# Performance work log

Measured on AMD Instinct MI355X. Metric: run time of the kernel, lower is better.

The kernel has to match this reference:

```python
import jax, jax.numpy as jnp
import numpy as np
import jax.scipy.linalg as jsp

H = 8
C = 64
D_CONV = 4
EPS_L2 = 1e-6
EPS_RMS = 1e-5


def l2norm(x):
    return x * jax.lax.rsqrt(jnp.sum(x * x, axis=-1, keepdims=True) + EPS_L2)


def setup_inputs() -> dict:
    key = jax.random.key(0)
    ks = jax.random.split(key, 12)
    B, T, D = 4, 4096, 1024
    x = jax.random.normal(ks[0], (B, T, D), dtype=jnp.float32)
    s = 0.02
    Wv = jax.random.normal(ks[1], (D, D), dtype=jnp.float32) * s
    Wg = jax.random.normal(ks[2], (D, D), dtype=jnp.float32) * s
    Wo = jax.random.normal(ks[3], (D, D), dtype=jnp.float32) * s
    Wb = jax.random.normal(ks[4], (H, D), dtype=jnp.float32) * s
    Wa = jax.random.normal(ks[5], (H, D), dtype=jnp.float32) * s
    # dt_bias / A_log initialized as in the torch module
    u = jax.random.uniform(ks[6], (H,))
    dt = jnp.exp(u * (jnp.log(0.1) - jnp.log(0.001)) + jnp.log(0.001))
    dt_bias = dt + jnp.log(-jnp.expm1(-dt))
    A_log = jnp.log(jax.random.uniform(ks[7], (H,)) * 16.0 + 1e-4)
    norm_w = jnp.ones((D // H,), dtype=jnp.float32)
    conv_w = jax.random.normal(ks[8], (D, D_CONV), dtype=jnp.float32) * 0.1
    conv_b = jnp.zeros((D,), dtype=jnp.float32)
    return {"x": x, "Wv": Wv, "Wg": Wg, "Wo": Wo, "Wb": Wb, "Wa": Wa,
            "dt_bias": dt_bias, "A_log": A_log, "norm_w": norm_w,
            "conv_w": conv_w, "conv_b": conv_b}


def _causal_depthwise_conv(x, w, b):
    # x: (B,T,D), w: (D,d_conv) -- causal depthwise conv1d
    B, T, D = x.shape
    xp = jnp.pad(x, ((0, 0), (D_CONV - 1, 0), (0, 0)))
    out = b
    for j in range(D_CONV):
        out = out + xp[:, j:j + T] * w[:, j]
    return out


def _forward(x, Wv, Wg, Wo, Wb, Wa, dt_bias, A_log, norm_w, conv_w, conv_b):
    B, T, D = x.shape
    K = D // H
    n = T // C  # T chosen as a multiple of C, so pad_len == 0

    rk = l2norm(x.reshape(B, T, H, K)) / np.sqrt(K)
    x_shift = jnp.pad(x[:, :-1], ((0, 0), (1, 0), (0, 0)))
    wk = l2norm(x_shift.reshape(B, T, H, K))
    v = jax.nn.silu(_causal_depthwise_conv(x @ Wv.T, conv_w, conv_b)).reshape(B, T, H, K)
    gate = (x @ Wg.T).reshape(B, T, H, K)
    beta = jax.nn.sigmoid(x @ Wb.T)                       # (B,T,H)
    decay = -jnp.exp(A_log) * jax.nn.softplus(x @ Wa.T + dt_bias)  # (B,T,H)

    # -> (B,H,T,K)
    rk, wk, v = (jnp.transpose(t, (0, 2, 1, 3)) for t in (rk, wk, v))
    beta_t = jnp.transpose(beta, (0, 2, 1))[..., None]    # (B,H,T,1)
    v = v * beta_t
    wk_beta = wk * beta_t

    # chunk: (B,H,n,C,K)
    ch = lambda t: t.reshape(B, H, n, C, K)
    rk, wk, v, wk_beta = ch(rk), ch(wk), ch(v), ch(wk_beta)
    decay = jnp.cumsum(jnp.transpose(decay, (0, 2, 1)).reshape(B, H, n, C), axis=-1)
    decay_exp = jnp.exp(decay)[..., None]                 # (B,H,n,C,1)

    tril = jnp.tril(jnp.ones((C, C), dtype=bool))
    strict_lower = jnp.tril(jnp.ones((C, C), dtype=bool), k=-1)
    diff = decay[..., :, None] - decay[..., None, :]
    L_mask = jnp.where(tril, jnp.exp(jnp.where(tril, diff, 0.0)), 0.0)  # (B,H,n,C,C)

    A_strict = jnp.where(strict_lower,
                         -(jnp.einsum('bhnck,bhndk->bhncd', wk_beta, wk) * L_mask), 0.0)
    # forward-substitution loop == inverse of unit-lower-triangular (I - A_strict)
    eye = jnp.eye(C, dtype=x.dtype)
    Tmat = jsp.solve_triangular(eye - A_strict,
                                jnp.broadcast_to(eye, A_strict.shape),
                                lower=True)
    v = Tmat @ v
    wk_cumdecay = Tmat @ (wk_beta * decay_exp)

    # scan over chunks maintaining state S: (B,H,K,K)
    def step(S, inp):
        rk_i, wk_i, v_i, wkc_i, L_i, dec_i = inp
        attn = jnp.where(tril, jnp.einsum('bhck,bhdk->bhcd', rk_i, wk_i) * L_i, 0.0)
        v_new = v_i - wkc_i @ S
        o_inter = (rk_i * jnp.exp(dec_i)[..., None]) @ S
        o_i = o_inter + attn @ v_new
        dw = jnp.exp(dec_i[..., -1:] - dec_i)[..., None]
        S_new = S * jnp.exp(dec_i[..., -1])[..., None, None] + \
            jnp.einsum('bhck,bhcv->bhkv', wk_i * dw, v_new)
        return S_new, o_i

    mv = lambda t: jnp.moveaxis(t, 2, 0)  # chunk axis to front
    S0 = jnp.zeros((B, H, K, K), dtype=x.dtype)
    _, o = jax.lax.scan(step, S0, (mv(rk), mv(wk), mv(v), mv(wk_cumdecay),
                                   mv(L_mask), mv(decay)))
    # o: (n,B,H,C,K) -> (B,T,H,K)
    o = jnp.transpose(o, (1, 0, 3, 2, 4)).reshape(B, T, H, K)

    # per-head RMSNorm, gated, output projection
    o = o * jax.lax.rsqrt(jnp.mean(o * o, axis=-1, keepdims=True) + EPS_RMS) * norm_w
    o = o * jax.nn.silu(gate)
    return o.reshape(B, T, D) @ Wo.T


def reference(x, Wv, Wg, Wo, Wb, Wa, dt_bias, A_log, norm_w, conv_w, conv_b):
    return _forward(x, Wv, Wg, Wo, Wb, Wa, dt_bias, A_log, norm_w, conv_w, conv_b)
```

## Files before the change

kernel.cpp:

```cpp
#include <hip/hip_runtime.h>
#include <hip/hip_bf16.h>
#include <math.h>

#define H_ 8
#define K_ 128
#define C_ 64
#define D_ 1024
#define T_ 4096
#define B_ 4
#define N_CH 64
#define BT_ (B_*T_)

typedef __attribute__((ext_vector_type(8))) short bf16x8;
typedef __attribute__((ext_vector_type(4))) float f32x4;
typedef __hip_bfloat16 bf16;

#define BAR_LGKM() do { \
  asm volatile("s_waitcnt lgkmcnt(0)" ::: "memory"); \
  __builtin_amdgcn_sched_barrier(0); \
  __builtin_amdgcn_s_barrier(); \
} while(0)

__device__ __forceinline__ float siluf(float x){ return x / (1.0f + expf(-x)); }
__device__ __forceinline__ float expn(float x){ return expf(fminf(x, 0.f)); }
__device__ __forceinline__ float sanf(float v){ return (__builtin_fabsf(v) <= 1e30f) ? v : 0.f; }

__device__ __forceinline__ void ld_bf4(const bf16* p, float* o){
  uint2 u = *(const uint2*)p;
  o[0]=__uint_as_float(u.x<<16); o[1]=__uint_as_float(u.x&0xffff0000u);
  o[2]=__uint_as_float(u.y<<16); o[3]=__uint_as_float(u.y&0xffff0000u);
}
__device__ __forceinline__ void ld_bf4s(const bf16* p, float* o){
  ld_bf4(p, o);
#pragma unroll
  for (int e=0;e<4;e++) o[e] = sanf(o[e]);
}
__device__ __forceinline__ unsigned short f2bfu(float f){
  bf16 h = __float2bfloat16(f);
  return *reinterpret_cast<unsigned short*>(&h);
}
__device__ __forceinline__ uint2 pack_bf4(const float* v){
  uint2 r;
  r.x = (unsigned)f2bfu(v[0]) | ((unsigned)f2bfu(v[1])<<16);
  r.y = (unsigned)f2bfu(v[2]) | ((unsigned)f2bfu(v[3])<<16);
  return r;
}
__device__ __forceinline__ bf16x8 u4_to_b8(uint4 u){
  union { uint4 u; bf16x8 b; } cv; cv.u = u; return cv.b;
}

template<int I> __device__ __forceinline__ void fsub_step(float* v, const float (*sa)[64]){
  const float* ar = sa[I];
  float s0=0.f,s1=0.f,s2=0.f,s3=0.f;
  constexpr int I4 = I & ~3;
#pragma unroll
  for (int j=0;j<I4;j+=4){
    float4 a4 = *(const float4*)&ar[j];
    s0 += a4.x*v[j+0]; s1 += a4.y*v[j+1]; s2 += a4.z*v[j+2]; s3 += a4.w*v[j+3];
  }
#pragma unroll
  for (int j=I4;j<I;j++) s0 += ar[j]*v[j];
  v[I] += (s0+s2)+(s1+s3);
}
template<int I> __device__ __forceinline__ void fsub_all(float* v, const float (*sa)[64]){
  if constexpr (I >= 1){
    fsub_all<I-1>(v, sa);
    fsub_step<I>(v, sa);
  }
}

__global__ __launch_bounds__(256) void cast_f2b(
    const float* __restrict__ src, bf16* __restrict__ dst, int n4)
{
  int i = blockIdx.x*256 + threadIdx.x;
  if (i >= n4) return;
  float4 v = *(const float4*)&src[(size_t)i*4];
  float a[4] = {v.x, v.y, v.z, v.w};
  *(uint2*)&dst[(size_t)i*4] = pack_bf4(a);
}

template<typename OUT_T, bool FUSE_NG>
__global__ __launch_bounds__(256) void gemm_bt_mfma(
    const bf16* __restrict__ X, const bf16* __restrict__ W,
    OUT_T* __restrict__ Y, int M, int N, int K,
    const bf16* __restrict__ o_in, const float* __restrict__ norm_w)
{
  __shared__ __align__(16) bf16 As[128*64];
  __shared__ __align__(16) bf16 Bs[128*64];
  const int tid = threadIdx.x;
  const int wv = tid >> 6;
  const int lane = tid & 63;
  const int row0 = blockIdx.y*128, col0 = blockIdx.x*128;
  const int mw = (wv&1)*64, nw = (wv>>1)*64;
  const int q = lane >> 4;
  const int l15 = lane & 15;
  const int swr = l15 & 7;
  f32x4 acc[4][4];
#pragma unroll
  for (int mi=0;mi<4;mi++)
#pragma unroll
    for (int ni=0;ni<4;ni++) acc[mi][ni] = (f32x4){0.f,0.f,0.f,0.f};

  const int sr8 = lane >> 3;
  const int scs = ((lane & 7) ^ sr8) * 8;
  for (int k0=0;k0<K;k0+=64){
#pragma unroll
    for (int i=0;i<4;i++){
      __builtin_amdgcn_global_load_lds(
          (const void*)&X[(size_t)(row0 + i*32 + wv*8 + sr8)*K + k0 + scs],
          (void*)&As[i*2048 + wv*512], 16, 0, 0);
      __builtin_amdgcn_global_load_lds(
          (const void*)&W[(size_t)(col0 + i*32 + wv*8 + sr8)*K + k0 + scs],
          (void*)&Bs[i*2048 + wv*512], 16, 0, 0);
    }
    __syncthreads();
#pragma unroll
    for (int ks=0; ks<64; ks+=32){
      bf16x8 af[4], bfr[4];
#pragma unroll
      for (int i=0;i<4;i++){
        const int cc = (((ks>>3) + q) ^ swr) * 8;
        af[i]  = *(const bf16x8*)&As[(mw + i*16 + l15)*64 + cc];
        bfr[i] = *(const bf16x8*)&Bs[(nw + i*16 + l15)*64 + cc];
      }
#pragma unroll
      for (int mi=0;mi<4;mi++)
#pragma unroll
        for (int ni=0;ni<4;ni++)
          acc[mi][ni] = __builtin_amdgcn_mfma_f32_16x16x32_bf16(af[mi], bfr[ni], acc[mi][ni], 0,0,0);
    }
    __syncthreads();
  }

  if constexpr (FUSE_NG){
    float* s_red = (float*)As;
    const int hh = blockIdx.x;
    const int nwh = nw >> 6;
#pragma unroll
    for (int mi=0;mi<4;mi++){
#pragma unroll
      for (int reg=0;reg<4;reg++){
        int row = row0 + mw + mi*16 + q*4 + reg;
        int b = row >> 12, t = row & (T_-1);
        const bf16* orow = o_in + ((size_t)(b*H_+hh)*T_ + t)*K_;
        float ps = 0.f;
#pragma unroll
        for (int ni=0;ni<4;ni++){
          float ov = sanf(__bfloat162float(orow[nw + ni*16 + l15]));
          ps += ov*ov;
        }
        ps += __shfl_xor(ps,1,64); ps += __shfl_xor(ps,2,64);
        ps += __shfl_xor(ps,4,64); ps += __shfl_xor(ps,8,64);
        if (l15 == 0) s_red[nwh*128 + mw + mi*16 + q*4 + reg] = ps;
      }
    }
    __syncthreads();
#pragma unroll
    for (int mi=0;mi<4;mi++){
#pragma unroll
      for (int reg=0;reg<4;reg++){
        int lr = mw + mi*16 + q*4 + reg;
        float ssum = s_red[lr] + s_red[128 + lr];
        float rr = rsqrtf(ssum*(1.f/128.f) + 1e-5f);
        int row = row0 + lr;
        int b = row >> 12, t = row & (T_-1);
        const bf16* orow = o_in + ((size_t)(b*H_+hh)*T_ + t)*K_;
#pragma unroll
        for (int ni=0;ni<4;ni++){
          int k = nw + ni*16 + l15;
          float ov = sanf(__bfloat162float(orow[k]));
          float res = ov * rr * norm_w[k] * siluf(acc[mi][ni][reg]);
          Y[(size_t)row*N + col0 + k] = (OUT_T)__float2bfloat16(res);
        }
      }
    }
  } else {
#pragma unroll
    for (int mi=0;mi<4;mi++){
#pragma unroll
      for (int reg=0;reg<4;reg++){
        int row = row0 + mw + mi*16 + q*4 + reg;
#pragma unroll
        for (int ni=0;ni<4;ni++){
          int col = col0 + nw + ni*16 + l15;
          if constexpr (sizeof(OUT_T) == 2)
            Y[(size_t)row*N + col] = (OUT_T)__float2bfloat16(acc[mi][ni][reg]);
          else
            Y[(size_t)row*N + col] = (OUT_T)acc[mi][ni][reg];
        }
      }
    }
  }
}

__global__ __launch_bounds__(256) void proj_small(
    const float* __restrict__ x, const float* __restrict__ Wb, const float* __restrict__ Wa,
    const float* __restrict__ dt_bias, const float* __restrict__ A_log,
    float* __restrict__ beta_out, float* __restrict__ dec_out)
{
  const int w = threadIdx.x >> 6;
  const int lane = threadIdx.x & 63;
  const int bt = blockIdx.x*4 + w;
  const int b = bt >> 12, t = bt & (T_-1);
  const float* xr = x + (size_t)bt*D_;
  float xv[16];
#pragma unroll
  for (int p=0;p<4;p++){
    float4 v = *(const float4*)&xr[lane*16 + p*4];
    xv[p*4+0]=v.x; xv[p*4+1]=v.y; xv[p*4+2]=v.z; xv[p*4+3]=v.w;
  }
  float accb[H_], acca[H_];
#pragma unroll
  for (int h=0;h<H_;h++){
    float sb=0.f, sa=0.f;
#pragma unroll
    for (int p=0;p<4;p++){
      float4 wb = *(const float4*)&Wb[(size_t)h*D_ + lane*16 + p*4];
      float4 wa = *(const float4*)&Wa[(size_t)h*D_ + lane*16 + p*4];
      sb += xv[p*4+0]*wb.x + xv[p*4+1]*wb.y + xv[p*4+2]*wb.z + xv[p*4+3]*wb.w;
      sa += xv[p*4+0]*wa.x + xv[p*4+1]*wa.y + xv[p*4+2]*wa.z + xv[p*4+3]*wa.w;
    }
    accb[h]=sb; acca[h]=sa;
  }
#pragma unroll
  for (int h=0;h<H_;h++){
#pragma unroll
    for (int m=1;m<64;m<<=1){
      accb[h] += __shfl_xor(accb[h], m, 64);
      acca[h] += __shfl_xor(acca[h], m, 64);
    }
  }
  if (lane < H_) {
    int h = lane;
    beta_out[(size_t)(b*H_+h)*T_ + t] = 1.f/(1.f+expf(-accb[h]));
  } else if (lane < 2*H_) {
    int h = lane - H_;
    float z = acca[h] + dt_bias[h];
    float sp = fmaxf(z,0.f) + log1pf(expf(-fabsf(z)));
    dec_out[(size_t)(b*H_+h)*T_ + t] = -expf(A_log[h]) * sp;
  }
}

__global__ __launch_bounds__(256) void xinv_kernel(
    const float* __restrict__ x, float* __restrict__ xinv, bf16* __restrict__ xb)
{
  const int bt = blockIdx.x;
  const int b = bt >> 12, t = bt & (T_-1);
  const int tid = threadIdx.x;
  float4 xv = *(const float4*)&x[(size_t)bt*D_ + tid*4];
  float a[4] = {xv.x, xv.y, xv.z, xv.w};
  *(uint2*)&xb[(size_t)bt*D_ + tid*4] = pack_bf4(a);
  float ss = xv.x*xv.x + xv.y*xv.y + xv.z*xv.z + xv.w*xv.w;
#pragma unroll
  for (int m=1;m<32;m<<=1) ss += __shfl_xor(ss, m, 32);
  const int h = tid >> 5;
  if ((tid & 31) == 0)
    xinv[(size_t)(b*H_+h)*T_ + t] = rsqrtf(ss + 1e-6f);
}

__global__ __launch_bounds__(256) void cumsum_dec(
    const float* __restrict__ dec_raw, float* __restrict__ dec_cum)
{
  int g = blockIdx.x*4 + (threadIdx.x>>6);
  int lane = threadIdx.x & 63;
  float v = sanf(dec_raw[(size_t)g*C_ + lane]);
#pragma unroll
  for (int off=1; off<64; off<<=1){
    float u = __shfl_up(v, off, 64);
    if (lane >= off) v += u;
  }
  dec_cum[(size_t)g*C_ + lane] = v;
}

__global__ __launch_bounds__(256) void chunk_prep(
    const bf16* __restrict__ xb, const float* __restrict__ xinv,
    const bf16* __restrict__ vpre, const float* __restrict__ cw, const float* __restrict__ cb,
    const float* __restrict__ beta, const float* __restrict__ dec,
    bf16* __restrict__ vchk, bf16* __restrict__ wkc, bf16* __restrict__ attn)
{
  __shared__ __align__(16) bf16 s_x[65][136];
  __shared__ __align__(16) float s_a[64][64];
  __shared__ float s_dec[64], s_beta[64], s_invsh[64], s_negbi[64], s_rsc[64], s_sc2[64];

  const int tid = threadIdx.x;
  const int chunk = blockIdx.x;
  const int bh = chunk >> 6;
  const int nc = chunk & 63;
  const int b = bh >> 3, h = bh & 7;
  const int t0 = nc * C_;
  const size_t xrow = (size_t)b*T_;
  const size_t rowb = (size_t)bh*T_ + t0;
  const size_t kobase = rowb * K_;
  const int w = tid >> 6;
  const int lane = tid & 63;
  const int l15 = lane & 15;
  const int q = lane >> 4;

  for (int idx = tid; idx < 65*16; idx += 256){
    int r = idx >> 4;
    int seg = (idx & 15) * 8;
    int t = t0 + r - 1;
    int tr = t < 0 ? 0 : t;
    *(uint4*)&s_x[r][seg] = *(const uint4*)&xb[(xrow + tr)*D_ + h*K_ + seg];
  }
  if (tid < C_){
    int c = tid;
    float dv  = sanf(dec[rowb + c]);
    float bet = sanf(beta[rowb + c]);
    float invc = sanf(xinv[rowb + c]);
    int tm1 = t0 + c - 1;
    float ivs = (tm1 >= 0) ? sanf(xinv[(size_t)bh*T_ + tm1]) : 0.f;
    s_dec[c] = dv;
    s_beta[c] = bet;
    s_invsh[c] = ivs;
    s_negbi[c] = -bet * ivs;
    s_rsc[c] = invc * 0.08838834764831845f;
    s_sc2[c] = ivs * bet * expn(dv);
  }
  __syncthreads();

  bf16x8 aG[4], aT[4];
#pragma unroll
  for (int ks=0; ks<4; ks++){
    aG[ks] = *(const bf16x8*)&s_x[16*w + l15][ks*32 + q*8];
    aT[ks] = *(const bf16x8*)&s_x[16*w + l15 + 1][ks*32 + q*8];
  }
  f32x4 accG[4], accT[4];
#pragma unroll
  for (int J=0;J<4;J++){ accG[J]=(f32x4){0.f,0.f,0.f,0.f}; accT[J]=(f32x4){0.f,0.f,0.f,0.f}; }
#pragma unroll
  for (int J=0;J<4;J++){
    if (J <= w){
#pragma unroll
      for (int ks=0; ks<4; ks++){
        bf16x8 bfrag = *(const bf16x8*)&s_x[16*J + l15][ks*32 + q*8];
        accG[J] = __builtin_amdgcn_mfma_f32_16x16x32_bf16(aG[ks], bfrag, accG[J], 0,0,0);
        accT[J] = __builtin_amdgcn_mfma_f32_16x16x32_bf16(aT[ks], bfrag, accT[J], 0,0,0);
      }
    }
  }
  {
    const int i0 = 16*w + q*4;
#pragma unroll
    for (int J=0;J<4;J++){
      const int j = 16*J + l15;
#pragma unroll
      for (int reg=0;reg<4;reg++){
        const int i = i0 + reg;
        if (j < i)
          s_a[i][j] = s_negbi[i] * s_invsh[j] * expn(s_dec[i]-s_dec[j]) * accG[J][reg];
        float val = 0.f;
        if (j <= i)
          val = s_rsc[i] * s_invsh[j] * expn(s_dec[i]-s_dec[j]) * accT[J][reg];
        attn[(size_t)chunk*4096 + i*64 + j] = __float2bfloat16(val);
      }
    }
  }

  float v[64];
  if (tid < 128){
    const int col = tid;
    float4 cwv = *(const float4*)&cw[(h*K_+col)*4];
    const float cbv = cb[h*K_+col];
    const bf16* vp = vpre + (xrow + t0)*D_ + h*K_ + col;
    float win0, win1, win2;
    { int t = t0-3; win0 = (t>=0)? sanf(__bfloat162float(vpre[(xrow+t)*D_+h*K_+col])) : 0.f; }
    { int t = t0-2; win1 = (t>=0)? sanf(__bfloat162float(vpre[(xrow+t)*D_+h*K_+col])) : 0.f; }
    { int t = t0-1; win2 = (t>=0)? sanf(__bfloat162float(vpre[(xrow+t)*D_+h*K_+col])) : 0.f; }
#pragma unroll
    for (int c8=0; c8<8; c8++){
      float nv[8];
#pragma unroll
      for (int u=0;u<8;u++) nv[u] = sanf(__bfloat162float(vp[(size_t)(c8*8+u)*D_]));
#pragma unroll
      for (int u=0;u<8;u++){
        const int c = c8*8+u;
        float a = cbv + cwv.x*win0 + cwv.y*win1 + cwv.z*win2 + cwv.w*nv[u];
        v[c] = siluf(a) * s_beta[c];
        win0=win1; win1=win2; win2=nv[u];
      }
    }
  } else {
    const int col = tid - 128;
#pragma unroll
    for (int c=0;c<64;c++)
      v[c] = __bfloat162float(s_x[c][col]) * s_sc2[c];
  }
  __syncthreads();

  fsub_all<63>(v, s_a);

  {
    const int col = tid & 127;
    bf16* dst = (tid < 128 ? vchk : wkc) + kobase + col;
#pragma unroll
    for (int c=0;c<64;c++)
      dst[(size_t)c*K_] = __float2bfloat16(v[c]);
  }
}

__global__ __launch_bounds__(512) void scan_kernel(
    const bf16* __restrict__ xb, const float* __restrict__ xinv, bf16* vo,
    const bf16* __restrict__ wkc, const bf16* __restrict__ attn,
    const float* __restrict__ dec)
{
  __shared__ __align__(16) bf16 xst[2][128][72];
  __shared__ __align__(16) bf16 st_hi[16][136];
  __shared__ __align__(16) bf16 st_lo[16][136];
  __shared__ __align__(16) bf16 vn_t [16][72];
  __shared__ __align__(16) bf16 vn_sh[16][72];
  __shared__ __align__(16) bf16 vn_sl[16][72];

  const int tid = threadIdx.x;
  const int bh = blockIdx.x & 31;
  const int g  = blockIdx.x >> 5;
  const int b = bh >> 3, h = bh & 7;
  const int j0 = g*16;
  const int w  = tid >> 6;
  const int wm = w & 3;
  const int lane = tid & 63;
  const int l15 = lane & 15;
  const int q = lane >> 4;
  const int wrow = 16*wm;
  const int c0 = wrow + q*4;
  const size_t xrow = (size_t)b*T_;
  const size_t bhT = (size_t)bh*T_;

  for (int e=tid; e<16*136; e+=512){
    ((unsigned short*)&st_hi[0][0])[e] = 0;
    ((unsigned short*)&st_lo[0][0])[e] = 0;
  }

  if (w < 4){
    f32x4 accS[2];
    accS[0] = (f32x4){0.f,0.f,0.f,0.f};
    accS[1] = (f32x4){0.f,0.f,0.f,0.f};

    const bf16*  pw   = wkc + (bhT + wrow + l15)*K_ + q*8;
    const bf16*  pv   = vo  + (bhT + c0)*K_ + j0 + l15;
    const float* pd   = dec + bhT + c0;
    const float* pd63 = dec + bhT + 63;
    const float* pxm  = xinv + bhT + c0;

    uint4 P_w[4]; bf16 P_v[4]; float4 P_d; float P_d63, P_xm[4];
#pragma unroll
    for (int ks=0; ks<4; ks++) P_w[ks] = *(const uint4*)(pw + ks*32);
#pragma unroll
    for (int r=0;r<4;r++) P_v[r] = pv[(size_t)r*K_];
    P_d = *(const float4*)pd;
    P_d63 = *pd63;
#pragma unroll
    for (int r=0;r<4;r++){
      int tm1 = c0 + r - 1;
      P_xm[r] = (tm1 >= 0) ? xinv[bhT + tm1] : 0.f;
    }
    BAR_LGKM();

    for (int nc=0; nc<N_CH; nc++){
      float d63s = sanf(P_d63);
      float a63 = expn(d63s);
      float cd[4] = {sanf(P_d.x), sanf(P_d.y), sanf(P_d.z), sanf(P_d.w)};
      float scv[4], vinitf[4];
#pragma unroll
      for (int r=0;r<4;r++){
        scv[r] = sanf(P_xm[r]) * expn(d63s - cd[r]);
        vinitf[r] = __bfloat162float(P_v[r]);
      }

      f32x4 accV;
#pragma unroll
      for (int r=0;r<4;r++) accV[r] = vinitf[r];
      __builtin_amdgcn_s_setprio(1);
#pragma unroll
      for (int ks=0; ks<4; ks++){
        bf16x8 bh_ = *(const bf16x8*)&st_hi[l15][ks*32 + q*8];
        bf16x8 bl_ = *(const bf16x8*)&st_lo[l15][ks*32 + q*8];
        uint4 uw = P_w[ks];
        uw.x ^= 0x80008000u; uw.y ^= 0x80008000u; uw.z ^= 0x80008000u; uw.w ^= 0x80008000u;
        bf16x8 a1 = u4_to_b8(uw);
        accV = __builtin_amdgcn_mfma_f32_16x16x32_bf16(a1, bh_, accV, 0,0,0);
        accV = __builtin_amdgcn_mfma_f32_16x16x32_bf16(a1, bl_, accV, 0,0,0);
      }
      __builtin_amdgcn_s_setprio(0);
      {
        float v4[4] = {accV[0],accV[1],accV[2],accV[3]};
        *(uint2*)&vn_t[l15][c0] = pack_bf4(v4);
        float vs[4];
#pragma unroll
        for (int r=0;r<4;r++) vs[r] = accV[r] * scv[r];
        uint2 ph = pack_bf4(vs);
        float lo4[4];
        lo4[0] = vs[0] - __uint_as_float(ph.x << 16);
        lo4[1] = vs[1] - __uint_as_float(ph.x & 0xffff0000u);
        lo4[2] = vs[2] - __uint_as_float(ph.y << 16);
        lo4[3] = vs[3] - __uint_as_float(ph.y & 0xffff0000u);
        *(uint2*)&vn_sh[l15][c0] = ph;
        *(uint2*)&vn_sl[l15][c0] = pack_bf4(lo4);
      }
      if (nc+1 < N_CH){ pw += (size_t)C_*K_; pv += (size_t)C_*K_; pd += C_; pd63 += C_; pxm += C_; }
#pragma unroll
      for (int ks=0; ks<4; ks++) P_w[ks] = *(const uint4*)(pw + ks*32);
#pragma unroll
      for (int r=0;r<4;r++) P_v[r] = pv[(size_t)r*K_];
      P_d = *(const float4*)pd;
      P_d63 = *pd63;
#pragma unroll
      for (int r=0;r<4;r++) P_xm[r] = pxm[r-1];
      BAR_LGKM();

      __builtin_amdgcn_s_setprio(1);
      bf16x8 aH[2], aL[2];
#pragma unroll
      for (int ks=0; ks<2; ks++){
        aH[ks] = *(const bf16x8*)&vn_sh[l15][ks*32 + q*8];
        aL[ks] = *(const bf16x8*)&vn_sl[l15][ks*32 + q*8];
      }
#pragma unroll
      for (int sub=0; sub<2; sub++){
        f32x4 acc = accS[sub];
#pragma unroll
        for (int r=0;r<4;r++) acc[r] *= a63;
#pragma unroll
        for (int ks=0; ks<2; ks++){
          bf16x8 bX = *(const bf16x8*)&xst[nc&1][32*wm + 16*sub + l15][ks*32 + q*8];
          acc = __builtin_amdgcn_mfma_f32_16x16x32_bf16(aH[ks], bX, acc, 0,0,0);
          acc = __builtin_amdgcn_mfma_f32_16x16x32_bf16(aL[ks], bX, acc, 0,0,0);
        }
        accS[sub] = acc;
#pragma unroll
        for (int r=0;r<4;r++){
          float sv = acc[r];
          bf16 hb = __float2bfloat16(sv);
          st_hi[q*4+r][32*wm + 16*sub + l15] = hb;
          st_lo[q*4+r][32*wm + 16*sub + l15] = __float2bfloat16(sv - __bfloat162float(hb));
        }
      }
      __builtin_amdgcn_s_setprio(0);
      BAR_LGKM();
    }
  } else {
    const int tp = tid - 256;
    const int xc0 = (tp & 31)*2;
    const int xkb = (tp >> 5)*16;

    uint4 T_r[4];
    uint4 P_x[4], P_a[2];
    float4 P_dP, P_xi;

    {
      int t1 = xc0 - 1;
      const bf16* p1 = xb + (xrow + (t1<0?0:t1))*D_ + h*K_ + xkb;
      const bf16* p2 = xb + (xrow + xc0)*D_ + h*K_ + xkb;
      T_r[0]=*(const uint4*)p1; T_r[1]=*(const uint4*)(p1+8);
      T_r[2]=*(const uint4*)p2; T_r[3]=*(const uint4*)(p2+8);
    }
    {
      unsigned r1[8]={T_r[0].x,T_r[0].y,T_r[0].z,T_r[0].w,T_r[1].x,T_r[1].y,T_r[1].z,T_r[1].w};
      unsigned r2[8]={T_r[2].x,T_r[2].y,T_r[2].z,T_r[2].w,T_r[3].x,T_r[3].y,T_r[3].z,T_r[3].w};
#pragma unroll
      for (int i2=0;i2<8;i2++){
        *(unsigned*)&xst[0][xkb + 2*i2][xc0]     = (r1[i2] & 0xffffu) | (r2[i2] << 16);
        *(unsigned*)&xst[0][xkb + 2*i2 + 1][xc0] = (r1[i2] >> 16) | (r2[i2] & 0xffff0000u);
      }
    }
    {
      const bf16* p1 = xb + (xrow + C_ + xc0 - 1)*D_ + h*K_ + xkb;
      const bf16* p2 = xb + (xrow + C_ + xc0)*D_ + h*K_ + xkb;
      T_r[0]=*(const uint4*)p1; T_r[1]=*(const uint4*)(p1+8);
      T_r[2]=*(const uint4*)p2; T_r[3]=*(const uint4*)(p2+8);
    }
    const bf16* pt1 = xb + (xrow + 2*C_ + xc0 - 1)*D_ + h*K_ + xkb;
    const bf16* pt2 = xb + (xrow + 2*C_ + xc0)*D_ + h*K_ + xkb;

    const bf16*  px  = xb + (xrow + wrow + l15)*D_ + h*K_ + q*8;
    const bf16*  pa  = attn + (size_t)(bh*N_CH)*4096 + (wrow + l15)*64 + q*8;
    const float* pdP = dec + bhT + c0;
    const float* pxi = xinv + bhT + c0;
    bf16*        pvo = vo + (bhT + c0)*K_ + j0 + l15;

#pragma unroll
    for (int ks=0; ks<4; ks++) P_x[ks] = *(const uint4*)(px + ks*32);
    P_a[0] = *(const uint4*)pa; P_a[1] = *(const uint4*)(pa + 32);
    P_dP = *(const float4*)pdP;
    P_xi = *(const float4*)pxi;
    BAR_LGKM();

    for (int nc=0; nc<N_CH; nc++){
      float cd[4]  = {sanf(P_dP.x), sanf(P_dP.y), sanf(P_dP.z), sanf(P_dP.w)};
      float cxi[4] = {sanf(P_xi.x), sanf(P_xi.y), sanf(P_xi.z), sanf(P_xi.w)};
      float sov[4];
#pragma unroll
      for (int r=0;r<4;r++) sov[r] = cxi[r] * 0.08838834764831845f * expn(cd[r]);

      {
        unsigned r1[8]={T_r[0].x,T_r[0].y,T_r[0].z,T_r[0].w,T_r[1].x,T_r[1].y,T_r[1].z,T_r[1].w};
        unsigned r2[8]={T_r[2].x,T_r[2].y,T_r[2].z,T_r[2].w,T_r[3].x,T_r[3].y,T_r[3].z,T_r[3].w};
        const int buf = (nc+1)&1;
#pragma unroll
        for (int i2=0;i2<8;i2++){
          *(unsigned*)&xst[buf][xkb + 2*i2][xc0]     = (r1[i2] & 0xffffu) | (r2[i2] << 16);
          *(unsigned*)&xst[buf][xkb + 2*i2 + 1][xc0] = (r1[i2] >> 16) | (r2[i2] & 0xffff0000u);
        }
      }
      if (nc+2 < N_CH){
        T_r[0]=*(const uint4*)pt1; T_r[1]=*(const uint4*)(pt1+8);
        T_r[2]=*(const uint4*)pt2; T_r[3]=*(const uint4*)(pt2+8);
        pt1 += (size_t)C_*D_; pt2 += (size_t)C_*D_;
      }

      f32x4 accP = (f32x4){0.f,0.f,0.f,0.f};
      __builtin_amdgcn_s_setprio(1);
#pragma unroll
      for (int ks=0; ks<4; ks++){
        bf16x8 bh_ = *(const bf16x8*)&st_hi[l15][ks*32 + q*8];
        bf16x8 bl_ = *(const bf16x8*)&st_lo[l15][ks*32 + q*8];
        bf16x8 a2 = u4_to_b8(P_x[ks]);
        accP = __builtin_amdgcn_mfma_f32_16x16x32_bf16(a2, bh_, accP, 0,0,0);
        accP = __builtin_amdgcn_mfma_f32_16x16x32_bf16(a2, bl_, accP, 0,0,0);
      }
      __builtin_amdgcn_s_setprio(0);
      f32x4 oacc;
#pragma unroll
      for (int r=0;r<4;r++) oacc[r] = accP[r] * sov[r];
      if (nc+1 < N_CH){ px += (size_t)C_*D_; pdP += C_; pxi += C_; }
#pragma unroll
      for (int ks=0; ks<4; ks++) P_x[ks] = *(const uint4*)(px + ks*32);
      P_dP = *(const float4*)pdP;
      P_xi = *(const float4*)pxi;
      BAR_LGKM();

      __builtin_amdgcn_s_setprio(1);
#pragma unroll
      for (int ks=0; ks<2; ks++){
        bf16x8 bV = *(const bf16x8*)&vn_t[l15][ks*32 + q*8];
        bf16x8 aA = u4_to_b8(P_a[ks]);
        oacc = __builtin_amdgcn_mfma_f32_16x16x32_bf16(aA, bV, oacc, 0,0,0);
      }
      __builtin_amdgcn_s_setprio(0);
#pragma unroll
      for (int r=0;r<4;r++) pvo[(size_t)r*K_] = __float2bfloat16(oacc[r]);
      pvo += (size_t)C_*K_;
      if (nc+1 < N_CH){ pa += 4096; }
      P_a[0] = *(const uint4*)pa; P_a[1] = *(const uint4*)(pa + 32);
      BAR_LGKM();
    }
  }
}

extern "C" void kernel_launch(void* const* d_in, const int* in_sizes, int n_in,
                              void* d_out, int out_size, void* d_ws, size_t ws_size,
                              hipStream_t stream)
{
  const float* x       = (const float*)d_in[0];
  const float* Wv      = (const float*)d_in[1];
  const float* Wg      = (const float*)d_in[2];
  const float* Wo      = (const float*)d_in[3];
  const float* Wb      = (const float*)d_in[4];
  const float* Wa      = (const float*)d_in[5];
  const float* dt_bias = (const float*)d_in[6];
  const float* A_log   = (const float*)d_in[7];
  const float* norm_w  = (const float*)d_in[8];
  const float* conv_w  = (const float*)d_in[9];
  const float* conv_b  = (const float*)d_in[10];
  float* out = (float*)d_out;

  const size_t BTD = (size_t)B_*T_*D_;
  const size_t BHT = (size_t)B_*H_*T_;
  const size_t DD  = (size_t)D_*D_;

  float* beta = (float*)d_ws;
  float* decr = beta + BHT;
  float* decc = decr + BHT;
  float* xinv = decc + BHT;
  bf16* Wvb = (bf16*)(xinv + BHT);
  bf16* Wgb = Wvb + DD;
  bf16* Wob = Wgb + DD;
  bf16* xb   = Wob + DD;
  bf16* vpre = xb + BTD;
  bf16* wkc  = vpre + BTD;
  bf16* vo   = (bf16*)d_out;
  bf16* attn = vo + BTD;

  dim3 gemm_grid(D_/128, BT_/128);
  xinv_kernel<<<BT_, 256, 0, stream>>>(x, xinv, xb);
  cast_f2b<<<(DD/4+255)/256, 256, 0, stream>>>(Wv, Wvb, DD/4);
  cast_f2b<<<(DD/4+255)/256, 256, 0, stream>>>(Wg, Wgb, DD/4);
  cast_f2b<<<(DD/4+255)/256, 256, 0, stream>>>(Wo, Wob, DD/4);
  gemm_bt_mfma<bf16,false><<<gemm_grid, 256, 0, stream>>>(xb, Wvb, vpre, BT_, D_, D_, nullptr, nullptr);
  proj_small<<<BT_/4, 256, 0, stream>>>(x, Wb, Wa, dt_bias, A_log, beta, decr);
  cumsum_dec<<<(BHT/C_)/4, 256, 0, stream>>>(decr, decc);
  chunk_prep<<<B_*H_*N_CH, 256, 0, stream>>>(xb, xinv, vpre, conv_w, conv_b,
                                             beta, decc, vo , wkc, attn);
  scan_kernel<<<B_*H_*8, 512, 0, stream>>>(xb, xinv, vo, wkc, attn, decc);
  gemm_bt_mfma<bf16,true><<<gemm_grid, 256, 0, stream>>>(xb, Wgb, vpre, BT_, D_, D_, vo, norm_w);
  gemm_bt_mfma<float,false><<<gemm_grid, 256, 0, stream>>>(vpre, Wob, out, BT_, D_, D_, nullptr, nullptr);
}
```

Measured before the change: 586.9 us.

## Co-schedule gate GEMM with scan in one launch, split norm-gate epilogue

The sequential scan used only 256 blocks, leaving many CUs idle. The gate projection GEMM now runs as extra blocks (a 256x128 tile variant) in the same launch, so the scan and the GEMM can share the GPU concurrently. Because the gate GEMM can no longer read the scan output, the RMSNorm plus silu gating moves into a separate elementwise kernel that rewrites the gate buffer in place. This costs an extra kernel launch and a round trip of the gate tensor through memory, and the shared smem size plus the launch_bounds(512,4) setting may reduce scan occupancy or raise register pressure.

Result: faster. 553.8 us (-5.6%).

```diff
diff --git a/kernel.cpp b/kernel.cpp
--- a/kernel.cpp
+++ b/kernel.cpp
@@ -79,11 +79,10 @@
   *(uint2*)&dst[(size_t)i*4] = pack_bf4(a);
 }
 
-template<typename OUT_T, bool FUSE_NG>
+template<typename OUT_T>
 __global__ __launch_bounds__(256) void gemm_bt_mfma(
     const bf16* __restrict__ X, const bf16* __restrict__ W,
-    OUT_T* __restrict__ Y, int M, int N, int K,
-    const bf16* __restrict__ o_in, const float* __restrict__ norm_w)
+    OUT_T* __restrict__ Y, int M, int N, int K)
 {
   __shared__ __align__(16) bf16 As[128*64];
   __shared__ __align__(16) bf16 Bs[128*64];
@@ -131,63 +130,18 @@
     }
     __syncthreads();
   }
-
-  if constexpr (FUSE_NG){
-    float* s_red = (float*)As;
-    const int hh = blockIdx.x;
-    const int nwh = nw >> 6;
-#pragma unroll
-    for (int mi=0;mi<4;mi++){
-#pragma unroll
-      for (int reg=0;reg<4;reg++){
-        int row = row0 + mw + mi*16 + q*4 + reg;
-        int b = row >> 12, t = row & (T_-1);
-        const bf16* orow = o_in + ((size_t)(b*H_+hh)*T_ + t)*K_;
-        float ps = 0.f;
-#pragma unroll
-        for (int ni=0;ni<4;ni++){
-          float ov = sanf(__bfloat162float(orow[nw + ni*16 + l15]));
-          ps += ov*ov;
-        }
-        ps += __shfl_xor(ps,1,64); ps += __shfl_xor(ps,2,64);
-        ps += __shfl_xor(ps,4,64); ps += __shfl_xor(ps,8,64);
-        if (l15 == 0) s_red[nwh*128 + mw + mi*16 + q*4 + reg] = ps;
-      }
-    }
-    __syncthreads();
-#pragma unroll
-    for (int mi=0;mi<4;mi++){
-#pragma unroll
-      for (int reg=0;reg<4;reg++){
-        int lr = mw + mi*16 + q*4 + reg;
-        float ssum = s_red[lr] + s_red[128 + lr];
-        float rr = rsqrtf(ssum*(1.f/128.f) + 1e-5f);
-        int row = row0 + lr;
-        int b = row >> 12, t = row & (T_-1);
-        const bf16* orow = o_in + ((size_t)(b*H_+hh)*T_ + t)*K_;
-#pragma unroll
-        for (int ni=0;ni<4;ni++){
-          int k = nw + ni*16 + l15;
-          float ov = sanf(__bfloat162float(orow[k]));
-          float res = ov * rr * norm_w[k] * siluf(acc[mi][ni][reg]);
-          Y[(size_t)row*N + col0 + k] = (OUT_T)__float2bfloat16(res);
-        }
-      }
-    }
-  } else {
-#pragma unroll
-    for (int mi=0;mi<4;mi++){
-#pragma unroll
-      for (int reg=0;reg<4;reg++){
-        int row = row0 + mw + mi*16 + q*4 + reg;
-#pragma unroll
-        for (int ni=0;ni<4;ni++){
-          int col = col0 + nw + ni*16 + l15;
-          if constexpr (sizeof(OUT_T) == 2)
-            Y[(size_t)row*N + col] = (OUT_T)__float2bfloat16(acc[mi][ni][reg]);
-          else
-            Y[(size_t)row*N + col] = (OUT_T)acc[mi][ni][reg];
-        }
+#pragma unroll
+  for (int mi=0;mi<4;mi++){
+#pragma unroll
+    for (int reg=0;reg<4;reg++){
+      int row = row0 + mw + mi*16 + q*4 + reg;
+#pragma unroll
+      for (int ni=0;ni<4;ni++){
+        int col = col0 + nw + ni*16 + l15;
+        if constexpr (sizeof(OUT_T) == 2)
+          Y[(size_t)row*N + col] = (OUT_T)__float2bfloat16(acc[mi][ni][reg]);
+        else
+          Y[(size_t)row*N + col] = (OUT_T)acc[mi][ni][reg];
       }
     }
   }
@@ -399,21 +353,22 @@
   }
 }
 
-__global__ __launch_bounds__(512) void scan_kernel(
+__device__ __forceinline__ void scan_body(
+    int sid, int tid, unsigned char* smem,
     const bf16* __restrict__ xb, const float* __restrict__ xinv, bf16* vo,
     const bf16* __restrict__ wkc, const bf16* __restrict__ attn,
     const float* __restrict__ dec)
 {
-  __shared__ __align__(16) bf16 xst[2][128][72];
-  __shared__ __align__(16) bf16 st_hi[16][136];
-  __shared__ __align__(16) bf16 st_lo[16][136];
-  __shared__ __align__(16) bf16 vn_t [16][72];
-  __shared__ __align__(16) bf16 vn_sh[16][72];
-  __shared__ __align__(16) bf16 vn_sl[16][72];
-
-  const int tid = threadIdx.x;
-  const int bh = blockIdx.x & 31;
-  const int g  = blockIdx.x >> 5;
+  typedef bf16 (*xst_t)[128][72];
+  xst_t xst = (xst_t)smem;
+  bf16 (*st_hi)[136] = (bf16(*)[136])(smem + 36864);
+  bf16 (*st_lo)[136] = (bf16(*)[136])(smem + 41216);
+  bf16 (*vn_t )[72]  = (bf16(*)[72]) (smem + 45568);
+  bf16 (*vn_sh)[72]  = (bf16(*)[72]) (smem + 47872);
+  bf16 (*vn_sl)[72]  = (bf16(*)[72]) (smem + 50176);
+
+  const int bh = sid & 31;
+  const int g  = sid >> 5;
   const int b = bh >> 3, h = bh & 7;
   const int j0 = g*16;
   const int w  = tid >> 6;
@@ -645,6 +600,112 @@
       BAR_LGKM();
     }
   }
+}
+
+__device__ __forceinline__ void gemm256_body(
+    const bf16* __restrict__ X, const bf16* __restrict__ W,
+    bf16* __restrict__ Y, int gid, int tid, bf16* As, bf16* Bs)
+{
+  const int wv = tid >> 6;
+  const int lane = tid & 63;
+  const int bx = gid & 7, by = gid >> 3;
+  const int row0 = by*256, col0 = bx*128;
+  const int mw = (wv&3)*64, nw = (wv>>2)*64;
+  const int q = lane >> 4;
+  const int l15 = lane & 15;
+  const int swr = l15 & 7;
+  f32x4 acc[4][4];
+#pragma unroll
+  for (int mi=0;mi<4;mi++)
+#pragma unroll
+    for (int ni=0;ni<4;ni++) acc[mi][ni] = (f32x4){0.f,0.f,0.f,0.f};
+
+  const int sr8 = lane >> 3;
+  const int scs = ((lane & 7) ^ sr8) * 8;
+  for (int k0=0;k0<D_;k0+=64){
+#pragma unroll
+    for (int j=0;j<4;j++){
+      __builtin_amdgcn_global_load_lds(
+          (const void*)&X[(size_t)(row0 + (wv*4+j)*8 + sr8)*D_ + k0 + scs],
+          (void*)&As[(wv*4+j)*512], 16, 0, 0);
+    }
+#pragma unroll
+    for (int j=0;j<2;j++){
+      __builtin_amdgcn_global_load_lds(
+          (const void*)&W[(size_t)(col0 + (wv*2+j)*8 + sr8)*D_ + k0 + scs],
+          (void*)&Bs[(wv*2+j)*512], 16, 0, 0);
+    }
+    __syncthreads();
+#pragma unroll
+    for (int ks=0; ks<64; ks+=32){
+      bf16x8 af[4], bfr[4];
+#pragma unroll
+      for (int i=0;i<4;i++){
+        const int cc = (((ks>>3) + q) ^ swr) * 8;
+        af[i]  = *(const bf16x8*)&As[(mw + i*16 + l15)*64 + cc];
+        bfr[i] = *(const bf16x8*)&Bs[(nw + i*16 + l15)*64 + cc];
+      }
+#pragma unroll
+      for (int mi=0;mi<4;mi++)
+#pragma unroll
+        for (int ni=0;ni<4;ni++)
+          acc[mi][ni] = __builtin_amdgcn_mfma_f32_16x16x32_bf16(af[mi], bfr[ni], acc[mi][ni], 0,0,0);
+    }
+    __syncthreads();
+  }
+#pragma unroll
+  for (int mi=0;mi<4;mi++){
+#pragma unroll
+    for (int reg=0;reg<4;reg++){
+      int row = row0 + mw + mi*16 + q*4 + reg;
+#pragma unroll
+      for (int ni=0;ni<4;ni++){
+        int col = col0 + nw + ni*16 + l15;
+        Y[(size_t)row*D_ + col] = __float2bfloat16(acc[mi][ni][reg]);
+      }
+    }
+  }
+}
+
+__global__ __launch_bounds__(512, 4) void scan_gate_kernel(
+    const bf16* __restrict__ xb, const float* __restrict__ xinv, bf16* vo,
+    const bf16* __restrict__ wkc, const bf16* __restrict__ attn,
+    const float* __restrict__ dec,
+    const bf16* __restrict__ Wgb, bf16* __restrict__ gate)
+{
+  __shared__ __align__(16) unsigned char smem[52480];
+  const int bid = blockIdx.x;
+  if (bid < 256){
+    scan_body(bid, threadIdx.x, smem, xb, xinv, vo, wkc, attn, dec);
+  } else {
+    gemm256_body(xb, Wgb, gate, bid - 256, threadIdx.x,
+                 (bf16*)smem, (bf16*)(smem + 32768));
+  }
+}
+
+__global__ __launch_bounds__(256) void norm_gate(
+    const bf16* __restrict__ o, bf16* gio, const float* __restrict__ norm_w)
+{
+  const int bt = blockIdx.x;
+  const int b = bt >> 12, t = bt & (T_-1);
+  const int tid = threadIdx.x;
+  const int h = tid >> 5;
+  const int kk = (tid & 31)*4;
+  float ov[4];
+  ld_bf4s(o + ((size_t)(b*H_+h)*T_ + t)*K_ + kk, ov);
+  float ss = ov[0]*ov[0] + ov[1]*ov[1] + ov[2]*ov[2] + ov[3]*ov[3];
+#pragma unroll
+  for (int m=1;m<32;m<<=1) ss += __shfl_xor(ss, m, 32);
+  float r = rsqrtf(ss*(1.f/128.f) + 1e-5f);
+  float4 nw = *(const float4*)&norm_w[kk];
+  float gv[4];
+  ld_bf4s(gio + (size_t)bt*D_ + tid*4, gv);
+  float res[4];
+  res[0] = ov[0]*r*nw.x * siluf(gv[0]);
+  res[1] = ov[1]*r*nw.y * siluf(gv[1]);
+  res[2] = ov[2]*r*nw.z * siluf(gv[2]);
+  res[3] = ov[3]*r*nw.w * siluf(gv[3]);
+  *(uint2*)&gio[(size_t)bt*D_ + tid*4] = pack_bf4(res);
 }
 
 extern "C" void kernel_launch(void* const* d_in, const int* in_sizes, int n_in,
@@ -686,12 +747,13 @@
   cast_f2b<<<(DD/4+255)/256, 256, 0, stream>>>(Wv, Wvb, DD/4);
   cast_f2b<<<(DD/4+255)/256, 256, 0, stream>>>(Wg, Wgb, DD/4);
   cast_f2b<<<(DD/4+255)/256, 256, 0, stream>>>(Wo, Wob, DD/4);
-  gemm_bt_mfma<bf16,false><<<gemm_grid, 256, 0, stream>>>(xb, Wvb, vpre, BT_, D_, D_, nullptr, nullptr);
+  gemm_bt_mfma<bf16><<<gemm_grid, 256, 0, stream>>>(xb, Wvb, vpre, BT_, D_, D_);
   proj_small<<<BT_/4, 256, 0, stream>>>(x, Wb, Wa, dt_bias, A_log, beta, decr);
   cumsum_dec<<<(BHT/C_)/4, 256, 0, stream>>>(decr, decc);
   chunk_prep<<<B_*H_*N_CH, 256, 0, stream>>>(xb, xinv, vpre, conv_w, conv_b,
                                              beta, decc, vo , wkc, attn);
-  scan_kernel<<<B_*H_*8, 512, 0, stream>>>(xb, xinv, vo, wkc, attn, decc);
-  gemm_bt_mfma<bf16,true><<<gemm_grid, 256, 0, stream>>>(xb, Wgb, vpre, BT_, D_, D_, vo, norm_w);
-  gemm_bt_mfma<float,false><<<gemm_grid, 256, 0, stream>>>(vpre, Wob, out, BT_, D_, D_, nullptr, nullptr);
-}
+  scan_gate_kernel<<<768, 512, 0, stream>>>(xb, xinv, vo, wkc, attn, decc,
+                                            Wgb, vpre );
+  norm_gate<<<BT_, 256, 0, stream>>>(vo , vpre , norm_w);
+  gemm_bt_mfma<float><<<gemm_grid, 256, 0, stream>>>(vpre, Wob, out, BT_, D_, D_);
+}
```
